# Performance work log

Measured on AMD Instinct MI355X. Metric: run time of the kernel, lower is better.

## Reference

```python
import jax, jax.numpy as jnp
import numpy as np

B, IN, OUT, K = 512, 65536, 16384, 32

def setup_inputs() -> dict:
    key = jax.random.key(0)
    k1, k2, k3 = jax.random.split(key, 3)
    x = jax.random.normal(k1, (B, IN), dtype=jnp.float32)
    indices = jax.random.randint(k2, (OUT, K), 0, IN, dtype=jnp.int32)
    weight = jax.random.normal(k3, (OUT, K), dtype=jnp.float32) * 0.1
    bias = jnp.zeros((OUT,), dtype=jnp.float32)
    return {"x": x, "indices": indices, "weight": weight, "bias": bias}

def reference(x, indices, weight, bias):
    # Gather per-output feature subsets: (B, OUT, K)
    x_sel = x[:, indices]
    # Weighted sum over K connections per output, plus bias: (B, OUT)
    out = jnp.einsum('bok,ok->bo', x_sel, weight) + bias
    return out
```

## Files before the change

### kernel.cpp

```cpp
#include <hip/hip_runtime.h>

#define B_DIM   512
#define IN_DIM  65536
#define OUT_DIM 16384
#define K_DIM   32

static __device__ __forceinline__ unsigned short f2bf(float f) {
    unsigned u = __builtin_bit_cast(unsigned, f);
    unsigned r = (u + 0x7FFFu + ((u >> 16) & 1u)) >> 16;
    return (unsigned short)r;
}

static __device__ __forceinline__ float fcomp(float4 v, int c) {
    switch (c & 3) { case 0: return v.x; case 1: return v.y; case 2: return v.z; default: return v.w; }
}

__global__ __launch_bounds__(256) void transpose_bf16_k(const float* __restrict__ x,
                                                        unsigned short* __restrict__ xT) {
    const int c0 = blockIdx.x * 16;
    const int t  = threadIdx.x;
    #pragma unroll
    for (int h = 0; h < 2; ++h) {
        const int b = h * 256 + t;
        const float4* p = (const float4*)(x + (size_t)b * IN_DIM + c0);
        float4 v0 = p[0], v1 = p[1], v2 = p[2], v3 = p[3];
        #pragma unroll
        for (int c = 0; c < 16; ++c) {
            const float4 vv = (c < 4) ? v0 : (c < 8) ? v1 : (c < 12) ? v2 : v3;
            xT[(size_t)(c0 + c) * B_DIM + b] = f2bf(fcomp(vv, c));
        }
    }
}

#define SE 520

static __device__ __forceinline__ int icomp(int4 v, int c) {
    switch (c & 3) { case 0: return v.x; case 1: return v.y; case 2: return v.z; default: return v.w; }
}

__global__ __launch_bounds__(128, 4) void sparse_main(const unsigned short* __restrict__ xT,
                                                      const int*   __restrict__ idxp,
                                                      const float* __restrict__ wp,
                                                      const float* __restrict__ biasp,
                                                      float*       __restrict__ out) {
    __shared__ float lds[8][SE];
    const int o_blk = blockIdx.x * 8;
    const int t    = threadIdx.x;
    const int lane = t & 63;
    const int b4   = t * 4;

    const int4   iv = ((const int4*)  (idxp + o_blk * K_DIM))[lane];
    const float4 wv = ((const float4*)(wp   + o_blk * K_DIM))[lane];

    float4 acc[8];
    #pragma unroll
    for (int o = 0; o < 8; ++o) acc[o] = make_float4(0.f, 0.f, 0.f, 0.f);

    #pragma unroll
    for (int o = 0; o < 8; ++o) {
        #pragma unroll
        for (int k = 0; k < K_DIM; ++k) {
            const int flat = o * K_DIM + k;
            const int sl   = flat >> 2;
            const int   sidx = __builtin_amdgcn_readlane(icomp(iv, flat), sl);
            const float sw   = __int_as_float(
                __builtin_amdgcn_readlane(__float_as_int(fcomp(wv, flat)), sl));
            const uint2 u = *(const uint2*)(xT + ((size_t)sidx << 9) + b4);
            acc[o].x = fmaf(sw, __int_as_float(u.x << 16),          acc[o].x);
            acc[o].y = fmaf(sw, __int_as_float(u.x & 0xFFFF0000u),  acc[o].y);
            acc[o].z = fmaf(sw, __int_as_float(u.y << 16),          acc[o].z);
            acc[o].w = fmaf(sw, __int_as_float(u.y & 0xFFFF0000u),  acc[o].w);
        }
    }

    #pragma unroll
    for (int o = 0; o < 8; ++o) {
        const float bv = biasp[o_blk + o];
        acc[o].x += bv; acc[o].y += bv; acc[o].z += bv; acc[o].w += bv;
        *(float4*)(&lds[o][b4]) = acc[o];
    }
    __syncthreads();

    #pragma unroll
    for (int p = 0; p < 8; ++p) {
        const int q = p * 512 + t * 4;
        const int b = q >> 3;
        const int o = q & 7;
        float4 v;
        v.x = lds[o + 0][b];
        v.y = lds[o + 1][b];
        v.z = lds[o + 2][b];
        v.w = lds[o + 3][b];
        *(float4*)(out + (size_t)b * OUT_DIM + o_blk + o) = v;
    }
}

__global__ void sparse_fallback(const float* __restrict__ x,
                                const int*   __restrict__ idxp,
                                const float* __restrict__ wp,
                                const float* __restrict__ biasp,
                                float*       __restrict__ out) {
    const int i = blockIdx.x * blockDim.x + threadIdx.x;
    if (i >= B_DIM * OUT_DIM) return;
    const int b = i / OUT_DIM;
    const int o = i % OUT_DIM;
    float a = biasp[o];
    for (int k = 0; k < K_DIM; ++k) {
        const int idx = idxp[o * K_DIM + k];
        a = fmaf(wp[o * K_DIM + k], x[(size_t)b * IN_DIM + idx], a);
    }
    out[i] = a;
}

extern "C" void kernel_launch(void* const* d_in, const int* in_sizes, int n_in,
                              void* d_out, int out_size, void* d_ws, size_t ws_size,
                              hipStream_t stream) {
    const float* x       = (const float*)d_in[0];
    const int*   indices = (const int*)  d_in[1];
    const float* weight  = (const float*)d_in[2];
    const float* bias    = (const float*)d_in[3];
    float*       out     = (float*)d_out;

    const size_t need = (size_t)IN_DIM * B_DIM * sizeof(unsigned short);
    if (ws_size >= need) {
        unsigned short* xT = (unsigned short*)d_ws;
        transpose_bf16_k<<<IN_DIM / 16, 256, 0, stream>>>(x, xT);
        sparse_main<<<OUT_DIM / 8, 128, 0, stream>>>(xT, indices, weight, bias, out);
    } else {
        const int n = B_DIM * OUT_DIM;
        sparse_fallback<<<(n + 255) / 256, 256, 0, stream>>>(x, indices, weight, bias, out);
    }
}
```

Before: 326.9 us.

## Split outputs across four waves with 16-byte gathers and wider transpose tiles

The sparse kernel now uses 256 threads per block. Each of the four waves handles two of the block's eight outputs over the full batch, loading 8 bf16 values (16 bytes) per gathered row instead of 4, which cuts the serial readlane/gather chain per wave. The transpose kernel handles 32 columns per block with 512 threads, one batch row per thread, and output stores use nontemporal hints. The trade-off is more registers per lane for the wider loads, against more waves in flight and fewer load instructions.

```diff
diff --git a/kernel.cpp b/kernel.cpp
--- a/kernel.cpp
+++ b/kernel.cpp
@@ -4,6 +4,8 @@
 #define IN_DIM  65536
 #define OUT_DIM 16384
 #define K_DIM   32
+
+typedef float nfloat4 __attribute__((ext_vector_type(4)));
 
 static __device__ __forceinline__ unsigned short f2bf(float f) {
     unsigned u = __builtin_bit_cast(unsigned, f);
@@ -15,30 +17,23 @@
     switch (c & 3) { case 0: return v.x; case 1: return v.y; case 2: return v.z; default: return v.w; }
 }
 
-__global__ __launch_bounds__(256) void transpose_bf16_k(const float* __restrict__ x,
+__global__ __launch_bounds__(512) void transpose_bf16_k(const float* __restrict__ x,
                                                         unsigned short* __restrict__ xT) {
-    const int c0 = blockIdx.x * 16;
-    const int t  = threadIdx.x;
+    const int c0 = blockIdx.x * 32;
+    const int b  = threadIdx.x;
+    const float4* p = (const float4*)(x + (size_t)b * IN_DIM + c0);
+    float4 v[8];
     #pragma unroll
-    for (int h = 0; h < 2; ++h) {
-        const int b = h * 256 + t;
-        const float4* p = (const float4*)(x + (size_t)b * IN_DIM + c0);
-        float4 v0 = p[0], v1 = p[1], v2 = p[2], v3 = p[3];
-        #pragma unroll
-        for (int c = 0; c < 16; ++c) {
-            const float4 vv = (c < 4) ? v0 : (c < 8) ? v1 : (c < 12) ? v2 : v3;
-            xT[(size_t)(c0 + c) * B_DIM + b] = f2bf(fcomp(vv, c));
-        }
+    for (int j = 0; j < 8; ++j) v[j] = p[j];
+    #pragma unroll
+    for (int c = 0; c < 32; ++c) {
+        xT[(size_t)(c0 + c) * B_DIM + b] = f2bf(fcomp(v[c >> 2], c));
     }
 }
 
 #define SE 520
 
-static __device__ __forceinline__ int icomp(int4 v, int c) {
-    switch (c & 3) { case 0: return v.x; case 1: return v.y; case 2: return v.z; default: return v.w; }
-}
-
-__global__ __launch_bounds__(128, 4) void sparse_main(const unsigned short* __restrict__ xT,
+__global__ __launch_bounds__(256, 8) void sparse_main(const unsigned short* __restrict__ xT,
                                                       const int*   __restrict__ idxp,
                                                       const float* __restrict__ wp,
                                                       const float* __restrict__ biasp,
@@ -46,52 +41,61 @@
     __shared__ float lds[8][SE];
     const int o_blk = blockIdx.x * 8;
     const int t    = threadIdx.x;
+    const int wid  = t >> 6;
     const int lane = t & 63;
-    const int b4   = t * 4;
+    const int b8   = lane * 8;
 
-    const int4   iv = ((const int4*)  (idxp + o_blk * K_DIM))[lane];
-    const float4 wv = ((const float4*)(wp   + o_blk * K_DIM))[lane];
+    const int   iv = idxp[o_blk * K_DIM + wid * 64 + lane];
+    const float wv = wp  [o_blk * K_DIM + wid * 64 + lane];
 
-    float4 acc[8];
+    float4 a0[2], a1[2];
     #pragma unroll
-    for (int o = 0; o < 8; ++o) acc[o] = make_float4(0.f, 0.f, 0.f, 0.f);
+    for (int oo = 0; oo < 2; ++oo) {
+        a0[oo] = make_float4(0.f, 0.f, 0.f, 0.f);
+        a1[oo] = make_float4(0.f, 0.f, 0.f, 0.f);
+    }
 
     #pragma unroll
-    for (int o = 0; o < 8; ++o) {
+    for (int oo = 0; oo < 2; ++oo) {
         #pragma unroll
         for (int k = 0; k < K_DIM; ++k) {
-            const int flat = o * K_DIM + k;
-            const int sl   = flat >> 2;
-            const int   sidx = __builtin_amdgcn_readlane(icomp(iv, flat), sl);
+            const int L = oo * 32 + k;
+            const int   sidx = __builtin_amdgcn_readlane(iv, L);
             const float sw   = __int_as_float(
-                __builtin_amdgcn_readlane(__float_as_int(fcomp(wv, flat)), sl));
-            const uint2 u = *(const uint2*)(xT + ((size_t)sidx << 9) + b4);
-            acc[o].x = fmaf(sw, __int_as_float(u.x << 16),          acc[o].x);
-            acc[o].y = fmaf(sw, __int_as_float(u.x & 0xFFFF0000u),  acc[o].y);
-            acc[o].z = fmaf(sw, __int_as_float(u.y << 16),          acc[o].z);
-            acc[o].w = fmaf(sw, __int_as_float(u.y & 0xFFFF0000u),  acc[o].w);
+                __builtin_amdgcn_readlane(__float_as_int(wv), L));
+            const uint4 u = *(const uint4*)(xT + ((size_t)sidx << 9) + b8);
+            a0[oo].x = fmaf(sw, __int_as_float(u.x << 16),          a0[oo].x);
+            a0[oo].y = fmaf(sw, __int_as_float(u.x & 0xFFFF0000u),  a0[oo].y);
+            a0[oo].z = fmaf(sw, __int_as_float(u.y << 16),          a0[oo].z);
+            a0[oo].w = fmaf(sw, __int_as_float(u.y & 0xFFFF0000u),  a0[oo].w);
+            a1[oo].x = fmaf(sw, __int_as_float(u.z << 16),          a1[oo].x);
+            a1[oo].y = fmaf(sw, __int_as_float(u.z & 0xFFFF0000u),  a1[oo].y);
+            a1[oo].z = fmaf(sw, __int_as_float(u.w << 16),          a1[oo].z);
+            a1[oo].w = fmaf(sw, __int_as_float(u.w & 0xFFFF0000u),  a1[oo].w);
         }
     }
 
     #pragma unroll
-    for (int o = 0; o < 8; ++o) {
-        const float bv = biasp[o_blk + o];
-        acc[o].x += bv; acc[o].y += bv; acc[o].z += bv; acc[o].w += bv;
-        *(float4*)(&lds[o][b4]) = acc[o];
+    for (int oo = 0; oo < 2; ++oo) {
+        const float bv = biasp[o_blk + wid * 2 + oo];
+        a0[oo].x += bv; a0[oo].y += bv; a0[oo].z += bv; a0[oo].w += bv;
+        a1[oo].x += bv; a1[oo].y += bv; a1[oo].z += bv; a1[oo].w += bv;
+        *(float4*)(&lds[wid * 2 + oo][b8])     = a0[oo];
+        *(float4*)(&lds[wid * 2 + oo][b8 + 4]) = a1[oo];
     }
     __syncthreads();
 
     #pragma unroll
-    for (int p = 0; p < 8; ++p) {
-        const int q = p * 512 + t * 4;
+    for (int p = 0; p < 4; ++p) {
+        const int q = p * 1024 + t * 4;
         const int b = q >> 3;
         const int o = q & 7;
-        float4 v;
+        nfloat4 v;
         v.x = lds[o + 0][b];
         v.y = lds[o + 1][b];
         v.z = lds[o + 2][b];
         v.w = lds[o + 3][b];
-        *(float4*)(out + (size_t)b * OUT_DIM + o_blk + o) = v;
+        __builtin_nontemporal_store(v, (nfloat4*)(out + (size_t)b * OUT_DIM + o_blk + o));
     }
 }
 
@@ -124,8 +128,8 @@
     const size_t need = (size_t)IN_DIM * B_DIM * sizeof(unsigned short);
     if (ws_size >= need) {
         unsigned short* xT = (unsigned short*)d_ws;
-        transpose_bf16_k<<<IN_DIM / 16, 256, 0, stream>>>(x, xT);
-        sparse_main<<<OUT_DIM / 8, 128, 0, stream>>>(xT, indices, weight, bias, out);
+        transpose_bf16_k<<<IN_DIM / 32, 512, 0, stream>>>(x, xT);
+        sparse_main<<<OUT_DIM / 8, 256, 0, stream>>>(xT, indices, weight, bias, out);
     } else {
         const int n = B_DIM * OUT_DIM;
         sparse_fallback<<<(n + 255) / 256, 256, 0, stream>>>(x, indices, weight, bias, out);
```

Result: slower. 498.5 us (+52.5%).
